# Performance work log

Hardware: AMD Instinct MI355X
Metric: run time of the kernel (lower is better)

Reference implementation:

```python
import jax, jax.numpy as jnp
import numpy as np

NEG_SLOPE = 0.2

def setup_inputs() -> dict:
    key = jax.random.key(0)
    ks = jax.random.split(key, 10)
    B, N, M, D = 4, 2048, 128, 64
    return {
        "feat_src": jax.random.normal(ks[0], (B, N, D), dtype=jnp.float32),
        "feat_dst": jax.random.normal(ks[1], (B, M, D), dtype=jnp.float32),
        "feat_edge": jax.random.uniform(ks[2], (B, N, M), dtype=jnp.float32),
        "adj": jax.random.randint(ks[3], (B, N, M), 0, 2, dtype=jnp.int32),
        "W_src": jax.random.normal(ks[4], (D, D), dtype=jnp.float32) * 0.1,
        "W_dst": jax.random.normal(ks[5], (D, D), dtype=jnp.float32) * 0.1,
        "W_edge": jax.random.normal(ks[6], (D, 1), dtype=jnp.float32) * 0.1,
        "attn_l": jax.random.normal(ks[7], (D,), dtype=jnp.float32) * 0.1,
        "attn_r": jax.random.normal(ks[8], (D,), dtype=jnp.float32) * 0.1,
        "attn_e": jax.random.normal(ks[9], (D,), dtype=jnp.float32) * 0.1,
    }

def reference(feat_src, feat_dst, feat_edge, adj, W_src, W_dst, W_edge, attn_l, attn_r, attn_e):
    # Linear projections (PyTorch Linear: x @ W.T)
    hs = feat_src @ W_src.T                     # (B,N,D)
    hd = feat_dst @ W_dst.T                     # (B,M,D)
    he = feat_edge[..., None] * W_edge[:, 0]    # (B,N,M,D): fc_edge on scalar edge feature
    # triple attention scores
    el = hs @ attn_l                            # (B,N)
    er = hd @ attn_r                            # (B,M)
    ee = jnp.einsum('bnmd,d->bnm', he, attn_e)  # (B,N,M)
    a = el[..., None] + ee + er[:, None, :]     # (B,N,M)
    e = jax.nn.leaky_relu(a, negative_slope=NEG_SLOPE)
    mask = adj == 1
    e_masked = jnp.where(mask, e, -jnp.inf)
    alpha = jax.nn.softmax(e_masked, axis=-2)   # softmax over source nodes N
    # weighted message aggregation: (edge_proj + src_proj) * alpha, summed over N
    msg = (he + hs[:, :, None, :]) * alpha[..., None]   # (B,N,M,D)
    aggregated = msg.sum(axis=1)                # (B,M,D)
    return jax.nn.sigmoid(aggregated)
```

## Files before the change

### kernel.cpp

```cpp
#include <hip/hip_runtime.h>
#include <math.h>

#define BB 4
#define NN 2048
#define MM 128
#define DD 64
#define NEG_SLOPE 0.2f

#define MT 16
#define NMT (MM / MT)
#define NSPL 16
#define NR (NN / NSPL)
#define PSTR 132
#define QSTR 68

__global__ __launch_bounds__(256, 3) void fused_kernel(
        const float* __restrict__ fs, const float* __restrict__ W_src,
        const float* __restrict__ attn_l,
        const float* __restrict__ fd, const float* __restrict__ W_dst,
        const float* __restrict__ attn_r,
        const float* __restrict__ W_edge, const float* __restrict__ attn_e,
        const float* __restrict__ fe, const int* __restrict__ adj,
        float* __restrict__ pacc, float* __restrict__ pdn) {
    int ns = blockIdx.x, mt = blockIdx.y, b = blockIdx.z;
    int n0 = ns * NR, m0 = mt * MT;
    int t = threadIdx.x, lane = t & 63;

    __shared__ __align__(16) float fsh[NR * DD];
    __shared__ __align__(16) float p_lds[MT * PSTR];
    __shared__ float el_lds[NR];
    __shared__ float er_lds[MT];
    __shared__ float vl[DD], ur[DD];
    __shared__ float dred[16][17], fred[16][17];
    __shared__ float ce_s;

    const float4* fs4 = (const float4*)(fs + ((size_t)(b * NN + n0)) * DD);
#pragma unroll 4
    for (int k = 0; k < 8; ++k)
        ((float4*)fsh)[t + k * 256] = fs4[t + k * 256];

    if (t < 64) {
        float a = 0.f;
#pragma unroll 8
        for (int d2 = 0; d2 < DD; ++d2) a += attn_l[d2] * W_src[d2 * DD + t];
        vl[t] = a;
    } else if (t < 128) {
        float a = 0.f;
#pragma unroll 8
        for (int d2 = 0; d2 < DD; ++d2) a += attn_r[d2] * W_dst[d2 * DD + lane];
        ur[lane] = a;
    } else if (t < 192) {
        float v = W_edge[lane] * attn_e[lane];
#pragma unroll
        for (int off = 32; off > 0; off >>= 1) v += __shfl_xor(v, off, 64);
        if (lane == 0) ce_s = v;
    }
    __syncthreads();

    if (t < NR) {
        int n = t;
        float a = 0.f;
#pragma unroll 8
        for (int j = 0; j < DD; ++j) {
            int k = (n + j) & 63;
            a += fsh[n * DD + k] * vl[k];
        }
        el_lds[n] = a;
    } else if (t < 128 + MT) {
        int m = t - 128;
        float a = 0.f;
        const float* fdp = fd + (size_t)(b * MM + m0 + m) * DD;
#pragma unroll 8
        for (int k = 0; k < DD; ++k) a += fdp[k] * ur[k];
        er_lds[m] = a;
    }
    __syncthreads();

    {
        int m = t & 15, h = t >> 4;
        float ce = ce_s;
        float er_m = er_lds[m];
        const float* fe_p = fe + ((size_t)(b * NN + n0)) * MM + m0 + m;
        const int* adj_p = adj + ((size_t)(b * NN + n0)) * MM + m0 + m;
        float dsum = 0.f, fsum = 0.f;
#pragma unroll 4
        for (int j = 0; j < 8; ++j) {
            int n = h + j * 16;
            float f = fe_p[(size_t)n * MM];
            int a = adj_p[(size_t)n * MM];
            float s = el_lds[n] + ce * f + er_m;
            s = s > 0.f ? s : NEG_SLOPE * s;
            float p = (a == 1) ? __expf(s) : 0.f;
            p_lds[m * PSTR + n] = p;
            dsum += p;
            fsum += f * p;
        }
        dred[h][m] = dsum;
        fred[h][m] = fsum;
    }
    __syncthreads();

    float acc[8][2];
    {
        int nq = t >> 6, mh = (t >> 5) & 1, kq = t & 31;
#pragma unroll
        for (int i = 0; i < 8; ++i) { acc[i][0] = 0.f; acc[i][1] = 0.f; }
        int rbase = mh * 8 * PSTR;
#pragma unroll 2
        for (int n4 = 0; n4 < 8; ++n4) {
            int nb = nq * 32 + n4 * 4;
            float2 h0 = *(const float2*)&fsh[(nb + 0) * DD + kq * 2];
            float2 h1 = *(const float2*)&fsh[(nb + 1) * DD + kq * 2];
            float2 h2 = *(const float2*)&fsh[(nb + 2) * DD + kq * 2];
            float2 h3 = *(const float2*)&fsh[(nb + 3) * DD + kq * 2];
#pragma unroll
            for (int mj = 0; mj < 8; ++mj) {
                float4 p4 = *(const float4*)&p_lds[rbase + mj * PSTR + nb];
                acc[mj][0] += p4.x * h0.x + p4.y * h1.x + p4.z * h2.x + p4.w * h3.x;
                acc[mj][1] += p4.x * h0.y + p4.y * h1.y + p4.z * h2.y + p4.w * h3.y;
            }
        }
    }
    __syncthreads();

    {
        int nq = t >> 6, mh = (t >> 5) & 1, kq = t & 31;
        float* part = fsh + nq * (MT * DD);
#pragma unroll
        for (int mj = 0; mj < 8; ++mj)
            *(float2*)&part[(mh * 8 + mj) * DD + kq * 2] =
                make_float2(acc[mj][0], acc[mj][1]);
    }
    __syncthreads();

    size_t pbase = (size_t)((b * NMT + mt) * NSPL + ns) * MT;
    {
        int m = t >> 4, ks = t & 15;
        float4 s0 = *(const float4*)&fsh[0 * MT * DD + m * DD + ks * 4];
        float4 s1 = *(const float4*)&fsh[1 * MT * DD + m * DD + ks * 4];
        float4 s2 = *(const float4*)&fsh[2 * MT * DD + m * DD + ks * 4];
        float4 s3 = *(const float4*)&fsh[3 * MT * DD + m * DD + ks * 4];
        float4 o;
        o.x = s0.x + s1.x + s2.x + s3.x;
        o.y = s0.y + s1.y + s2.y + s3.y;
        o.z = s0.z + s1.z + s2.z + s3.z;
        o.w = s0.w + s1.w + s2.w + s3.w;
        *(float4*)&pacc[(pbase + m) * DD + ks * 4] = o;
    }
    if (t < MT) {
        float ds2 = 0.f, fs2 = 0.f;
#pragma unroll
        for (int k = 0; k < 16; ++k) { ds2 += dred[k][t]; fs2 += fred[k][t]; }
        size_t q = (pbase + t) * 2;
        pdn[q] = ds2;
        pdn[q + 1] = fs2;
    }
}

__global__ __launch_bounds__(256) void finish_kernel(
        const float* __restrict__ pacc, const float* __restrict__ pdn,
        const float* __restrict__ W_src, const float* __restrict__ W_edge,
        float* __restrict__ out) {
    int mt = blockIdx.x, b = blockIdx.y;
    int m0 = mt * MT;
    int t = threadIdx.x;

    __shared__ __align__(16) float WT[DD * DD];
    __shared__ __align__(16) float q_tot[MT * QSTR];
    __shared__ float dn_tot[MT], sf_tot[MT];

#pragma unroll
    for (int i = 0; i < 16; ++i) {
        int idx = t + i * 256;
        int k = idx >> 6, d = idx & 63;
        WT[idx] = W_src[d * DD + k];
    }
    {
        int m = t >> 4, kq = t & 15;
        size_t base = (size_t)((b * NMT + mt) * NSPL) * MT;
        float4 s = make_float4(0.f, 0.f, 0.f, 0.f);
#pragma unroll
        for (int nsj = 0; nsj < NSPL; ++nsj) {
            float4 v = *(const float4*)&pacc[(base + nsj * MT + m) * DD + kq * 4];
            s.x += v.x; s.y += v.y; s.z += v.z; s.w += v.w;
        }
        *(float4*)&q_tot[m * QSTR + kq * 4] = s;
    }
    if (t < MT) {
        size_t base = (size_t)((b * NMT + mt) * NSPL) * MT;
        float ds2 = 0.f, fs2 = 0.f;
#pragma unroll
        for (int nsj = 0; nsj < NSPL; ++nsj) {
            size_t q = (base + nsj * MT + t) * 2;
            ds2 += pdn[q];
            fs2 += pdn[q + 1];
        }
        dn_tot[t] = ds2;
        sf_tot[t] = fs2;
    }
    __syncthreads();
    {
        int m = t >> 4, dq = t & 15;
        float4 r = make_float4(0.f, 0.f, 0.f, 0.f);
#pragma unroll 8
        for (int k = 0; k < DD; ++k) {
            float qv = q_tot[m * QSTR + k];
            float4 wv = *(const float4*)&WT[k * DD + dq * 4];
            r.x += wv.x * qv; r.y += wv.y * qv;
            r.z += wv.z * qv; r.w += wv.w * qv;
        }
        float inv = 1.f / dn_tot[m];
        float sfe = sf_tot[m];
        float4 we = *(const float4*)&W_edge[dq * 4];
        float4 o;
        o.x = 1.f / (1.f + __expf(-(we.x * sfe + r.x) * inv));
        o.y = 1.f / (1.f + __expf(-(we.y * sfe + r.y) * inv));
        o.z = 1.f / (1.f + __expf(-(we.z * sfe + r.z) * inv));
        o.w = 1.f / (1.f + __expf(-(we.w * sfe + r.w) * inv));
        *(float4*)&out[((size_t)(b * MM + m0 + m)) * DD + dq * 4] = o;
    }
}

extern "C" void kernel_launch(void* const* d_in, const int* in_sizes, int n_in,
                              void* d_out, int out_size, void* d_ws, size_t ws_size,
                              hipStream_t stream) {
    const float* feat_src  = (const float*)d_in[0];
    const float* feat_dst  = (const float*)d_in[1];
    const float* feat_edge = (const float*)d_in[2];
    const int*   adj       = (const int*)d_in[3];
    const float* W_src     = (const float*)d_in[4];
    const float* W_dst     = (const float*)d_in[5];
    const float* W_edge    = (const float*)d_in[6];
    const float* attn_l    = (const float*)d_in[7];
    const float* attn_r    = (const float*)d_in[8];
    const float* attn_e    = (const float*)d_in[9];
    float* out = (float*)d_out;

    float* ws   = (float*)d_ws;
    float* pacc = ws;
    float* pdn  = pacc + (size_t)BB * NMT * NSPL * MT * DD;

    fused_kernel<<<dim3(NSPL, NMT, BB), 256, 0, stream>>>(
        feat_src, W_src, attn_l, feat_dst, W_dst, attn_r,
        W_edge, attn_e, feat_edge, adj, pacc, pdn);
    finish_kernel<<<dim3(NMT, BB), 256, 0, stream>>>(
        pacc, pdn, W_src, W_edge, out);
}
```

Before: 19.84 us.

## Drop in-block partial reduction; write per-wave partials and reduce in finish kernel

The fused kernel no longer stages its four wave-level partial accumulators through shared memory with two barriers and an LDS reduction. Each wave now writes its partial directly to global workspace, and the finish kernel sums 64 partials per tile instead of 16. The vl/ur projection setup is split across all 256 threads in two halves, and the fd dot product is vectorized with float4 loads. The trade is four times more workspace writes and reads in exchange for fewer syncs and less LDS traffic in the main kernel.

```diff
diff --git a/kernel.cpp b/kernel.cpp
--- a/kernel.cpp
+++ b/kernel.cpp
@@ -24,13 +24,14 @@
         float* __restrict__ pacc, float* __restrict__ pdn) {
     int ns = blockIdx.x, mt = blockIdx.y, b = blockIdx.z;
     int n0 = ns * NR, m0 = mt * MT;
-    int t = threadIdx.x, lane = t & 63;
+    int t = threadIdx.x;
 
     __shared__ __align__(16) float fsh[NR * DD];
     __shared__ __align__(16) float p_lds[MT * PSTR];
+    __shared__ __align__(16) float vpart[2][DD];
+    __shared__ __align__(16) float upart[2][DD];
     __shared__ float el_lds[NR];
     __shared__ float er_lds[MT];
-    __shared__ float vl[DD], ur[DD];
     __shared__ float dred[16][17], fred[16][17];
     __shared__ float ce_s;
 
@@ -39,21 +40,31 @@
     for (int k = 0; k < 8; ++k)
         ((float4*)fsh)[t + k * 256] = fs4[t + k * 256];
 
-    if (t < 64) {
-        float a = 0.f;
-#pragma unroll 8
-        for (int d2 = 0; d2 < DD; ++d2) a += attn_l[d2] * W_src[d2 * DD + t];
-        vl[t] = a;
-    } else if (t < 128) {
-        float a = 0.f;
-#pragma unroll 8
-        for (int d2 = 0; d2 < DD; ++d2) a += attn_r[d2] * W_dst[d2 * DD + lane];
-        ur[lane] = a;
-    } else if (t < 192) {
-        float v = W_edge[lane] * attn_e[lane];
-#pragma unroll
-        for (int off = 32; off > 0; off >>= 1) v += __shfl_xor(v, off, 64);
-        if (lane == 0) ce_s = v;
+    {
+        int k = t & 63, half = (t >> 6) & 1;
+        if (t < 128) {
+            float a = 0.f;
+#pragma unroll
+            for (int j = 0; j < 32; ++j) {
+                int d2 = half * 32 + j;
+                a += attn_l[d2] * W_src[d2 * DD + k];
+            }
+            vpart[half][k] = a;
+        } else {
+            float a = 0.f;
+#pragma unroll
+            for (int j = 0; j < 32; ++j) {
+                int d2 = half * 32 + j;
+                a += attn_r[d2] * W_dst[d2 * DD + k];
+            }
+            upart[half][k] = a;
+        }
+        if (t < 64) {
+            float v = W_edge[t] * attn_e[t];
+#pragma unroll
+            for (int off = 32; off > 0; off >>= 1) v += __shfl_xor(v, off, 64);
+            if (t == 0) ce_s = v;
+        }
     }
     __syncthreads();
 
@@ -62,16 +73,22 @@
         float a = 0.f;
 #pragma unroll 8
         for (int j = 0; j < DD; ++j) {
-            int k = (n + j) & 63;
-            a += fsh[n * DD + k] * vl[k];
+            int kk = (n + j) & 63;
+            a += fsh[n * DD + kk] * (vpart[0][kk] + vpart[1][kk]);
         }
         el_lds[n] = a;
-    } else if (t < 128 + MT) {
-        int m = t - 128;
+    } else if (t < NR + MT) {
+        int m = t - NR;
         float a = 0.f;
-        const float* fdp = fd + (size_t)(b * MM + m0 + m) * DD;
-#pragma unroll 8
-        for (int k = 0; k < DD; ++k) a += fdp[k] * ur[k];
+        const float4* fd4 = (const float4*)(fd + (size_t)(b * MM + m0 + m) * DD);
+#pragma unroll
+        for (int k4 = 0; k4 < 16; ++k4) {
+            float4 f = fd4[k4];
+            float4 u0 = *(const float4*)&upart[0][k4 * 4];
+            float4 u1 = *(const float4*)&upart[1][k4 * 4];
+            a += f.x * (u0.x + u1.x) + f.y * (u0.y + u1.y) +
+                 f.z * (u0.z + u1.z) + f.w * (u0.w + u1.w);
+        }
         er_lds[m] = a;
     }
     __syncthreads();
@@ -100,9 +117,9 @@
     }
     __syncthreads();
 
-    float acc[8][2];
     {
         int nq = t >> 6, mh = (t >> 5) & 1, kq = t & 31;
+        float acc[8][2];
 #pragma unroll
         for (int i = 0; i < 8; ++i) { acc[i][0] = 0.f; acc[i][1] = 0.f; }
         int rbase = mh * 8 * PSTR;
@@ -120,38 +137,19 @@
                 acc[mj][1] += p4.x * h0.y + p4.y * h1.y + p4.z * h2.y + p4.w * h3.y;
             }
         }
-    }
-    __syncthreads();
-
-    {
-        int nq = t >> 6, mh = (t >> 5) & 1, kq = t & 31;
-        float* part = fsh + nq * (MT * DD);
-#pragma unroll
-        for (int mj = 0; mj < 8; ++mj)
-            *(float2*)&part[(mh * 8 + mj) * DD + kq * 2] =
+        size_t pbase = ((size_t)((b * NMT + mt) * NSPL + ns) * 4 + nq) * MT;
+#pragma unroll
+        for (int mj = 0; mj < 8; ++mj) {
+            int m = mh * 8 + mj;
+            *(float2*)&pacc[(pbase + m) * DD + kq * 2] =
                 make_float2(acc[mj][0], acc[mj][1]);
-    }
-    __syncthreads();
-
-    size_t pbase = (size_t)((b * NMT + mt) * NSPL + ns) * MT;
-    {
-        int m = t >> 4, ks = t & 15;
-        float4 s0 = *(const float4*)&fsh[0 * MT * DD + m * DD + ks * 4];
-        float4 s1 = *(const float4*)&fsh[1 * MT * DD + m * DD + ks * 4];
-        float4 s2 = *(const float4*)&fsh[2 * MT * DD + m * DD + ks * 4];
-        float4 s3 = *(const float4*)&fsh[3 * MT * DD + m * DD + ks * 4];
-        float4 o;
-        o.x = s0.x + s1.x + s2.x + s3.x;
-        o.y = s0.y + s1.y + s2.y + s3.y;
-        o.z = s0.z + s1.z + s2.z + s3.z;
-        o.w = s0.w + s1.w + s2.w + s3.w;
-        *(float4*)&pacc[(pbase + m) * DD + ks * 4] = o;
+        }
     }
     if (t < MT) {
         float ds2 = 0.f, fs2 = 0.f;
 #pragma unroll
         for (int k = 0; k < 16; ++k) { ds2 += dred[k][t]; fs2 += fred[k][t]; }
-        size_t q = (pbase + t) * 2;
+        size_t q = ((size_t)((b * NMT + mt) * NSPL + ns) * MT + t) * 2;
         pdn[q] = ds2;
         pdn[q + 1] = fs2;
     }
@@ -177,11 +175,11 @@
     }
     {
         int m = t >> 4, kq = t & 15;
-        size_t base = (size_t)((b * NMT + mt) * NSPL) * MT;
+        size_t base = (size_t)((b * NMT + mt) * NSPL) * 4;
         float4 s = make_float4(0.f, 0.f, 0.f, 0.f);
-#pragma unroll
-        for (int nsj = 0; nsj < NSPL; ++nsj) {
-            float4 v = *(const float4*)&pacc[(base + nsj * MT + m) * DD + kq * 4];
+#pragma unroll 8
+        for (int sj = 0; sj < NSPL * 4; ++sj) {
+            float4 v = *(const float4*)&pacc[((base + sj) * MT + m) * DD + kq * 4];
             s.x += v.x; s.y += v.y; s.z += v.z; s.w += v.w;
         }
         *(float4*)&q_tot[m * QSTR + kq * 4] = s;
@@ -238,7 +236,7 @@
 
     float* ws   = (float*)d_ws;
     float* pacc = ws;
-    float* pdn  = pacc + (size_t)BB * NMT * NSPL * MT * DD;
+    float* pdn  = pacc + (size_t)BB * NMT * NSPL * 4 * MT * DD;
 
     fused_kernel<<<dim3(NSPL, NMT, BB), 256, 0, stream>>>(
         feat_src, W_src, attn_l, feat_dst, W_dst, attn_r,
```

After: 25.56 us. 1.29x slower.
